# Performance work log

Hardware: AMD Instinct MI355X
Metric: run time of the kernel (lower is better)

Reference implementation:

```python
import jax, jax.numpy as jnp
import numpy as np

HIDDEN = 256
NUM_CLASSES = 25
INPUT_DIM = 76


def _lstm_layer(x, Wi, Wh, b):
    """Flax OptimizedLSTMCell semantics: gates [i, f, g, o], zero-init carry.
    x: [B, T, D]; Wi: [D, 4H]; Wh: [H, 4H]; b: [4H]. Returns hidden seq [B, T, H]."""
    B = x.shape[0]
    H = Wh.shape[0]
    c0 = jnp.zeros((B, H), x.dtype)
    h0 = jnp.zeros((B, H), x.dtype)

    def step(carry, xt):
        c, h = carry
        z = xt @ Wi + h @ Wh + b  # [B, 4H]
        i, f, g, o = jnp.split(z, 4, axis=-1)
        i = jax.nn.sigmoid(i)
        f = jax.nn.sigmoid(f)
        g = jnp.tanh(g)
        o = jax.nn.sigmoid(o)
        c = f * c + i * g
        h = o * jnp.tanh(c)
        return (c, h), h

    (_, _), ys = jax.lax.scan(step, (c0, h0), jnp.swapaxes(x, 0, 1))  # scan over time
    return jnp.swapaxes(ys, 0, 1)  # [B, T, H]


def setup_inputs() -> dict:
    key = jax.random.key(0)
    ks = jax.random.split(key, 9)
    B, T, D, H = 512, 512, INPUT_DIM, HIDDEN
    s_in = 1.0 / np.sqrt(D)
    s_h = 1.0 / np.sqrt(H)
    return {
        "x": jax.random.normal(ks[0], (B, T, D), jnp.float32),
        "Wi1": jax.random.normal(ks[1], (D, 4 * H), jnp.float32) * s_in,
        "Wh1": jax.random.normal(ks[2], (H, 4 * H), jnp.float32) * s_h,
        "b1": jnp.zeros((4 * H,), jnp.float32),
        "Wi2": jax.random.normal(ks[3], (H, 4 * H), jnp.float32) * s_h,
        "Wh2": jax.random.normal(ks[4], (H, 4 * H), jnp.float32) * s_h,
        "b2": jnp.zeros((4 * H,), jnp.float32),
        "Wd": jax.random.normal(ks[5], (H, NUM_CLASSES), jnp.float32) * s_h,
        "bd": jnp.zeros((NUM_CLASSES,), jnp.float32),
    }


def reference(x, Wi1, Wh1, b1, Wi2, Wh2, b2, Wd, bd):
    h1 = _lstm_layer(x, Wi1, Wh1, b1)   # [B, T, H]
    h2 = _lstm_layer(h1, Wi2, Wh2, b2)  # [B, T, H]
    feats = h2[:, -1]                   # dropout deterministic (eval mode)
    logits = feats @ Wd + bd            # [B, num_classes]
    return logits
```

## Files before the change

### kernel.cpp

```cpp
#include <hip/hip_runtime.h>

#define BB 512
#define TT 512
#define DD 76
#define HH 256
#define NC 25
#define NBLK 256
#define NTHREADS 512
#define BBHH (BB * HH)

#define K1 352
#define K2 512
#define WS1 360
#define WS2 520

typedef unsigned short u16;
typedef unsigned int u32;
typedef unsigned long long u64;
typedef __attribute__((ext_vector_type(8))) short bf16x8;
typedef __attribute__((ext_vector_type(4))) float f32x4;

__device__ __forceinline__ float bf2f(u16 v) {
  union { u32 u; float f; } c; c.u = ((u32)v) << 16; return c.f;
}
__device__ __forceinline__ u16 f2bf(float f) {
  union { u32 u; float f; } c; c.f = f;
  u32 r = c.u + 0x7FFFu + ((c.u >> 16) & 1u);
  return (u16)(r >> 16);
}
__device__ __forceinline__ void split2(float f, u16& h, u16& l) {
  u16 hh = f2bf(f);
  float r = f - bf2f(hh);
  h = hh; l = f2bf(r);
}
__device__ __forceinline__ float tanh_f(float v) {
  float e = __expf(2.0f * v);
  return 1.0f - 2.0f / (e + 1.0f);
}
__device__ __forceinline__ float gact(float v, bool is_tanh) {
  float e = __expf(is_tanh ? 2.0f * v : -v);
  float inv = 1.0f / (1.0f + e);
  return is_tanh ? 1.0f - 2.0f * inv : inv;
}

__device__ __forceinline__ u64 ald2(const u32* p) {
  return __hip_atomic_load((const u64*)p, __ATOMIC_RELAXED, __HIP_MEMORY_SCOPE_AGENT);
}
__device__ __forceinline__ u32 ald1(const u32* p) {
  return __hip_atomic_load(p, __ATOMIC_RELAXED, __HIP_MEMORY_SCOPE_AGENT);
}
__device__ __forceinline__ void ast1(u32* p, u32 v) {
  __hip_atomic_store(p, v, __ATOMIC_RELAXED, __HIP_MEMORY_SCOPE_AGENT);
}
__device__ __forceinline__ void ast2(u64* p, u64 v) {
  __hip_atomic_store(p, v, __ATOMIC_RELAXED, __HIP_MEMORY_SCOPE_AGENT);
}

__device__ __forceinline__ void wait_flags(const u32* fbase, u32 target) {
  if (threadIdx.x < 32) {
    const u32* p = fbase + threadIdx.x * 32;
    while (__hip_atomic_load(p, __ATOMIC_RELAXED, __HIP_MEMORY_SCOPE_AGENT) < target)
      __builtin_amdgcn_s_sleep(1);
  }
  __syncthreads();
}
__device__ __forceinline__ void post_flag(u32* slot, u32 val) {
  __syncthreads();
  if (threadIdx.x == 0) ast1(slot, val);
}

__device__ __forceinline__ bf16x8 hi8(const u64 w[4]) {
  union { u32 u[4]; bf16x8 v; } c;
#pragma unroll
  for (int i = 0; i < 4; ++i)
    c.u[i] = __builtin_amdgcn_perm((u32)(w[i] >> 32), (u32)w[i], 0x05040100u);
  return c.v;
}
__device__ __forceinline__ bf16x8 lo8(const u64 w[4]) {
  union { u32 u[4]; bf16x8 v; } c;
#pragma unroll
  for (int i = 0; i < 4; ++i)
    c.u[i] = __builtin_amdgcn_perm((u32)(w[i] >> 32), (u32)w[i], 0x07060302u);
  return c.v;
}

__device__ __forceinline__ void splitv8(const float* f, bf16x8& vh, bf16x8& vl) {
  union { u16 s[8]; bf16x8 v; } ch, cl;
#pragma unroll
  for (int i = 0; i < 8; ++i) { u16 h_, l_; split2(f[i], h_, l_); ch.s[i] = h_; cl.s[i] = l_; }
  vh = ch.v; vl = cl.v;
}

__global__ void repack_kernel(const float* __restrict__ Wi1, const float* __restrict__ Wh1,
                              const float* __restrict__ Wi2, const float* __restrict__ Wh2,
                              u16* __restrict__ w1hg, u16* __restrict__ w1lg,
                              u16* __restrict__ w2hg, u16* __restrict__ w2lg) {
  int idx = blockIdx.x * blockDim.x + threadIdx.x;
  const int N1 = 1024 * K1;
  if (idx < N1) {
    int c = idx / K1, k = idx - c * K1;
    int src = (c & 3) * HH + (c >> 2);
    float v = 0.f;
    if (k < HH) v = Wh1[k * 1024 + src];
    else if (k < HH + DD) v = Wi1[(k - HH) * 1024 + src];
    u16 h, l; split2(v, h, l);
    w1hg[idx] = h; w1lg[idx] = l;
  } else if (idx < N1 + 1024 * K2) {
    int d = idx - N1;
    int c = d >> 9, k = d & 511;
    int src = (c & 3) * HH + (c >> 2);
    float v = (k < HH) ? Wi2[k * 1024 + src] : Wh2[(k - HH) * 1024 + src];
    u16 h, l; split2(v, h, l);
    w2hg[d] = h; w2lg[d] = l;
  }
}

#define MFMA_CH6(AH, AL, PH0, PL0, PH1, PL1, KOFF, A0, B0, C0, A1, B1, C1)  \
  { bf16x8 b0h_ = *(const bf16x8*)((PH0) + (KOFF));                         \
    bf16x8 b0l_ = *(const bf16x8*)((PL0) + (KOFF));                         \
    bf16x8 b1h_ = *(const bf16x8*)((PH1) + (KOFF));                         \
    bf16x8 b1l_ = *(const bf16x8*)((PL1) + (KOFF));                         \
    A0 = __builtin_amdgcn_mfma_f32_16x16x32_bf16(AH, b0h_, A0, 0, 0, 0);    \
    B0 = __builtin_amdgcn_mfma_f32_16x16x32_bf16(AH, b0l_, B0, 0, 0, 0);    \
    C0 = __builtin_amdgcn_mfma_f32_16x16x32_bf16(AL, b0h_, C0, 0, 0, 0);    \
    A1 = __builtin_amdgcn_mfma_f32_16x16x32_bf16(AH, b1h_, A1, 0, 0, 0);    \
    B1 = __builtin_amdgcn_mfma_f32_16x16x32_bf16(AH, b1l_, B1, 0, 0, 0);    \
    C1 = __builtin_amdgcn_mfma_f32_16x16x32_bf16(AL, b1h_, C1, 0, 0, 0); }

#define GATES_ST(Z, CS, DST)                                                \
  { u32 hwv[4];                                                             \
    _Pragma("unroll")                                                       \
    for (int r = 0; r < 4; ++r) {                                           \
      float a_ = gact((Z)[r], gi == 2);                                     \
      float v1_ = __shfl_xor(a_, 1);                                        \
      float v2_ = __shfl_xor(a_, 2);                                        \
      float v3_ = __shfl_xor(a_, 3);                                        \
      float cn_ = v1_ * (CS)[r] + a_ * v2_;                                 \
      (CS)[r] = cn_;                                                        \
      float hv_ = v3_ * tanh_f(cn_);                                        \
      u16 hh_, hl_; split2(hv_, hh_, hl_);                                  \
      hwv[r] = (u32)hh_ | ((u32)hl_ << 16);                                 \
    }                                                                       \
    _Pragma("unroll")                                                       \
    for (int r = 0; r < 4; ++r) {                                           \
      int base_ = lane & 48;                                                \
      u32 w1_ = __shfl(hwv[r], base_ + 4);                                  \
      u32 w2_ = __shfl(hwv[r], base_ + 8);                                  \
      u32 w3_ = __shfl(hwv[r], base_ + 12);                                 \
      if (nl == 0) {                                                        \
        u64* dp_ = (u64*)((DST) + (size_t)(rbase + r) * HH + jt * 8 + kh * 4); \
        ast2(dp_,     (u64)hwv[r] | ((u64)w1_ << 32));                      \
        ast2(dp_ + 1, (u64)w2_    | ((u64)w3_ << 32));                      \
      }                                                                     \
    }                                                                       \
  }

#define LOAD_RW(RW, BASEPTR)                                                \
  { const u32* hp_ = (BASEPTR) + (size_t)arow * HH + kh * 128;              \
    _Pragma("unroll")                                                       \
    for (int i_ = 0; i_ < 4; ++i_) {                                        \
      const u32* p_ = hp_ + i_ * 32 + qd * 8;                               \
      (RW)[i_][0] = ald2(p_);     (RW)[i_][1] = ald2(p_ + 2);               \
      (RW)[i_][2] = ald2(p_ + 4); (RW)[i_][3] = ald2(p_ + 6);               \
    } }

__global__ __launch_bounds__(NTHREADS) void lstm_kernel(
    const float* __restrict__ x,
    const float* __restrict__ b1, const float* __restrict__ b2,
    const float* __restrict__ Wd, const float* __restrict__ bd,
    const u16* __restrict__ w1hg, const u16* __restrict__ w1lg,
    const u16* __restrict__ w2hg, const u16* __restrict__ w2lg,
    u32* __restrict__ h1w, u32* __restrict__ h2w,
    u32* __restrict__ flags,
    float* __restrict__ out)
{
  __shared__ u16 w1h[32 * WS1], w1l[32 * WS1];
  __shared__ u16 w2h[32 * WS2], w2l[32 * WS2];
  __shared__ float zx[2][8][64][4];

  const int tid = threadIdx.x;
  const int lane = tid & 63;
  const int wv = tid >> 6;
  const int m  = wv & 3;
  const int kh = wv >> 2;
  const int nl = lane & 15;
  const int qd = lane >> 4;
  const int bt = blockIdx.x & 7;
  const int jt = blockIdx.x >> 3;
  const int row0 = bt * 64;

  u32* fCp = flags + bt * 1024;
  u32* fCslot = fCp + jt * 32;

  for (int i = tid; i < 32 * (K1 / 2); i += NTHREADS) {
    int c = i / 176, kk = i - c * 176;
    ((u32*)&w1h[c * WS1])[kk] = ((const u32*)(w1hg + (size_t)(jt * 32 + c) * K1))[kk];
    ((u32*)&w1l[c * WS1])[kk] = ((const u32*)(w1lg + (size_t)(jt * 32 + c) * K1))[kk];
  }
  for (int i = tid; i < 32 * (K2 / 2); i += NTHREADS) {
    int c = i >> 8, kk = i & 255;
    ((u32*)&w2h[c * WS2])[kk] = ((const u32*)(w2hg + (size_t)(jt * 32 + c) * K2))[kk];
    ((u32*)&w2l[c * WS2])[kk] = ((const u32*)(w2lg + (size_t)(jt * 32 + c) * K2))[kk];
  }

  const int cg_col = jt * 32 + kh * 16 + nl;
  const int gi = cg_col & 3;
  const int rbase = row0 + m * 16 + qd * 4;
  const int arow = row0 + m * 16 + nl;

  float ab1[2], ab2[2];
#pragma unroll
  for (int tl = 0; tl < 2; ++tl) {
    int col = jt * 32 + tl * 16 + nl;
    float v1 = b1[(col & 3) * HH + (col >> 2)];
    float v2 = b2[(col & 3) * HH + (col >> 2)];
    ab1[tl] = (kh == 0) ? v1 : 0.f;
    ab2[tl] = (kh == 0) ? v2 : 0.f;
  }

  const u16* pB1h0 = w1h + nl * WS1;
  const u16* pB1l0 = w1l + nl * WS1;
  const u16* pB1h1 = w1h + (16 + nl) * WS1;
  const u16* pB1l1 = w1l + (16 + nl) * WS1;
  const u16* pB2h0 = w2h + nl * WS2;
  const u16* pB2l0 = w2l + nl * WS2;
  const u16* pB2h1 = w2h + (16 + nl) * WS2;
  const u16* pB2l1 = w2l + (16 + nl) * WS2;

  float cs1[4] = {0.f, 0.f, 0.f, 0.f}, cs2[4] = {0.f, 0.f, 0.f, 0.f};
  u64 rwh1[4][4], rw2[4][4];

  __syncthreads();

  {
    f32x4 aA0 = {ab1[0], ab1[0], ab1[0], ab1[0]};
    f32x4 aA1 = {ab1[1], ab1[1], ab1[1], ab1[1]};
    f32x4 aB0 = {0,0,0,0}, aB1 = {0,0,0,0}, aC0 = {0,0,0,0}, aC1 = {0,0,0,0};
    const float* xrow = x + (size_t)arow * TT * DD;
    if (kh == 0) {
#pragma unroll
      for (int ci = 0; ci < 2; ++ci) {
        float xv[8];
        float4 f0 = *(const float4*)(xrow + ci * 32 + qd * 8);
        float4 f1 = *(const float4*)(xrow + ci * 32 + qd * 8 + 4);
        xv[0]=f0.x; xv[1]=f0.y; xv[2]=f0.z; xv[3]=f0.w;
        xv[4]=f1.x; xv[5]=f1.y; xv[6]=f1.z; xv[7]=f1.w;
        bf16x8 xh, xl; splitv8(xv, xh, xl);
        const int koff = (8 + ci) * 32 + qd * 8;
        MFMA_CH6(xh, xl, pB1h0, pB1l0, pB1h1, pB1l1, koff, aA0, aB0, aC0, aA1, aB1, aC1)
      }
    } else {
      float xv[8] = {0,0,0,0,0,0,0,0};
      if (qd == 0) {
        float4 f0 = *(const float4*)(xrow + 64);
        float4 f1 = *(const float4*)(xrow + 68);
        xv[0]=f0.x; xv[1]=f0.y; xv[2]=f0.z; xv[3]=f0.w;
        xv[4]=f1.x; xv[5]=f1.y; xv[6]=f1.z; xv[7]=f1.w;
      } else if (qd == 1) {
        float4 f0 = *(const float4*)(xrow + 72);
        xv[0]=f0.x; xv[1]=f0.y; xv[2]=f0.z; xv[3]=f0.w;
      }
      bf16x8 xh, xl; splitv8(xv, xh, xl);
      const int koff = 10 * 32 + qd * 8;
      MFMA_CH6(xh, xl, pB1h0, pB1l0, pB1h1, pB1l1, koff, aA0, aB0, aC0, aA1, aB1, aC1)
    }
    f32x4 zk = (kh == 0) ? (aA0 + aB0 + aC0) : (aA1 + aB1 + aC1);
    f32x4 zo = (kh == 0) ? (aA1 + aB1 + aC1) : (aA0 + aB0 + aC0);
    *(f32x4*)&zx[1][wv][lane][0] = zo;
    __syncthreads();
    zk += *(const f32x4*)&zx[1][wv ^ 4][lane][0];
    GATES_ST(zk, cs1, h1w)
    post_flag(fCslot, 1u);
  }

#pragma unroll 1
  for (int t = 0; t < TT; ++t) {
    const u32* h1cw = h1w + (t & 1) * BBHH;
    u32* h1nw = h1w + ((t + 1) & 1) * BBHH;
    const u32* h2pw = h2w + ((t + 1) & 1) * BBHH;
    u32* h2cw = h2w + (t & 1) * BBHH;
    const bool doA = (t < TT - 1);

    f32x4 aA0 = {ab1[0], ab1[0], ab1[0], ab1[0]};
    f32x4 aA1 = {ab1[1], ab1[1], ab1[1], ab1[1]};
    f32x4 aB0 = {0,0,0,0}, aB1 = {0,0,0,0}, aC0 = {0,0,0,0}, aC1 = {0,0,0,0};
    f32x4 bA0 = {ab2[0], ab2[0], ab2[0], ab2[0]};
    f32x4 bA1 = {ab2[1], ab2[1], ab2[1], ab2[1]};
    f32x4 bB0 = {0,0,0,0}, bB1 = {0,0,0,0}, bC0 = {0,0,0,0}, bC1 = {0,0,0,0};

    float4 xf0, xf1, xf2, xf3;
    if (doA) {
      const float* xrow = x + ((size_t)arow * TT + (t + 1)) * DD;
      if (kh == 0) {
        xf0 = *(const float4*)(xrow + qd * 8);
        xf1 = *(const float4*)(xrow + qd * 8 + 4);
        xf2 = *(const float4*)(xrow + 32 + qd * 8);
        xf3 = *(const float4*)(xrow + 32 + qd * 8 + 4);
      } else {
        xf0 = make_float4(0,0,0,0); xf1 = make_float4(0,0,0,0);
        if (qd == 0) {
          xf0 = *(const float4*)(xrow + 64);
          xf1 = *(const float4*)(xrow + 68);
        } else if (qd == 1) {
          xf0 = *(const float4*)(xrow + 72);
        }
      }
    }

    wait_flags(fCp, (u32)(t + 1));

    LOAD_RW(rwh1, h1cw)
    if (t > 0) LOAD_RW(rw2, h2pw)

    if (doA) {
      float xv[8]; bf16x8 xh, xl;
      if (kh == 0) {
        xv[0]=xf0.x; xv[1]=xf0.y; xv[2]=xf0.z; xv[3]=xf0.w;
        xv[4]=xf1.x; xv[5]=xf1.y; xv[6]=xf1.z; xv[7]=xf1.w;
        splitv8(xv, xh, xl);
        MFMA_CH6(xh, xl, pB1h0, pB1l0, pB1h1, pB1l1, 8 * 32 + qd * 8,
                 aA0, aB0, aC0, aA1, aB1, aC1)
        xv[0]=xf2.x; xv[1]=xf2.y; xv[2]=xf2.z; xv[3]=xf2.w;
        xv[4]=xf3.x; xv[5]=xf3.y; xv[6]=xf3.z; xv[7]=xf3.w;
        splitv8(xv, xh, xl);
        MFMA_CH6(xh, xl, pB1h0, pB1l0, pB1h1, pB1l1, 9 * 32 + qd * 8,
                 aA0, aB0, aC0, aA1, aB1, aC1)
      } else {
        xv[0]=xf0.x; xv[1]=xf0.y; xv[2]=xf0.z; xv[3]=xf0.w;
        xv[4]=xf1.x; xv[5]=xf1.y; xv[6]=xf1.z; xv[7]=xf1.w;
        splitv8(xv, xh, xl);
        MFMA_CH6(xh, xl, pB1h0, pB1l0, pB1h1, pB1l1, 10 * 32 + qd * 8,
                 aA0, aB0, aC0, aA1, aB1, aC1)
      }
    }

#pragma unroll
    for (int i = 0; i < 4; ++i) {
      bf16x8 fh = hi8(rwh1[i]), fl = lo8(rwh1[i]);
      const int koff = (kh * 4 + i) * 32 + qd * 8;
      if (doA)
        MFMA_CH6(fh, fl, pB1h0, pB1l0, pB1h1, pB1l1, koff, aA0, aB0, aC0, aA1, aB1, aC1)
      MFMA_CH6(fh, fl, pB2h0, pB2l0, pB2h1, pB2l1, koff, bA0, bB0, bC0, bA1, bB1, bC1)
    }
    if (t > 0) {
#pragma unroll
      for (int i = 0; i < 4; ++i) {
        bf16x8 fh = hi8(rw2[i]), fl = lo8(rw2[i]);
        const int koff = (8 + kh * 4 + i) * 32 + qd * 8;
        MFMA_CH6(fh, fl, pB2h0, pB2l0, pB2h1, pB2l1, koff, bA0, bB0, bC0, bA1, bB1, bC1)
      }
    }

    f32x4 z2k = (kh == 0) ? (bA0 + bB0 + bC0) : (bA1 + bB1 + bC1);
    f32x4 z2o = (kh == 0) ? (bA1 + bB1 + bC1) : (bA0 + bB0 + bC0);
    *(f32x4*)&zx[0][wv][lane][0] = z2o;
    f32x4 z1k = {0,0,0,0};
    if (doA) {
      z1k = (kh == 0) ? (aA0 + aB0 + aC0) : (aA1 + aB1 + aC1);
      f32x4 z1o = (kh == 0) ? (aA1 + aB1 + aC1) : (aA0 + aB0 + aC0);
      *(f32x4*)&zx[1][wv][lane][0] = z1o;
    }
    __syncthreads();
    z2k += *(const f32x4*)&zx[0][wv ^ 4][lane][0];
    if (doA) {
      z1k += *(const f32x4*)&zx[1][wv ^ 4][lane][0];
      GATES_ST(z1k, cs1, h1nw)
    }
    GATES_ST(z2k, cs2, h2cw)
    post_flag(fCslot, (u32)(t + 2));
  }

  wait_flags(fCp, TT + 1);
  if (tid < 2 * NC) {
    int r = row0 + jt * 2 + tid / NC;
    int n = tid - (tid / NC) * NC;
    float s = bd[n];
    const u32* fw = h2w + BBHH + (size_t)r * HH;
#pragma unroll 8
    for (int k = 0; k < HH; ++k) {
      u32 w = ald1(fw + k);
      s += (bf2f((u16)w) + bf2f((u16)(w >> 16))) * Wd[k * NC + n];
    }
    out[r * NC + n] = s;
  }
}

extern "C" void kernel_launch(void* const* d_in, const int* in_sizes, int n_in,
                              void* d_out, int out_size, void* d_ws, size_t ws_size,
                              hipStream_t stream) {
  const float* x   = (const float*)d_in[0];
  const float* Wi1 = (const float*)d_in[1];
  const float* Wh1 = (const float*)d_in[2];
  const float* b1  = (const float*)d_in[3];
  const float* Wi2 = (const float*)d_in[4];
  const float* Wh2 = (const float*)d_in[5];
  const float* b2  = (const float*)d_in[6];
  const float* Wd  = (const float*)d_in[7];
  const float* bd  = (const float*)d_in[8];

  char* ws = (char*)d_ws;
  u32* h1w = (u32*)(ws);
  u32* h2w = (u32*)(ws + 1048576u);
  u16* w1hg = (u16*)(ws + 2097152u);
  u16* w1lg = (u16*)(ws + 2097152u + 720896u);
  u16* w2hg = (u16*)(ws + 2097152u + 2u * 720896u);
  u16* w2lg = (u16*)(ws + 2097152u + 2u * 720896u + 1048576u);
  u32* flags = (u32*)(ws + 5636096u);
  float* out = (float*)d_out;

  hipMemsetAsync((void*)flags, 0, 65536, stream);
  const int total = 1024 * K1 + 1024 * K2;
  repack_kernel<<<(total + 255) / 256, 256, 0, stream>>>(
      Wi1, Wh1, Wi2, Wh2, w1hg, w1lg, w2hg, w2lg);

  void* args[] = {
    (void*)&x, (void*)&b1, (void*)&b2, (void*)&Wd, (void*)&bd,
    (void*)&w1hg, (void*)&w1lg, (void*)&w2hg, (void*)&w2lg,
    (void*)&h1w, (void*)&h2w,
    (void*)&flags, (void*)&out
  };
  (void)hipLaunchCooperativeKernel((void*)lstm_kernel, dim3(NBLK),
                                   dim3(NTHREADS), args, 0, stream);
}
```

Baseline: 5.481 ms.

## Split LSTM work over 512 cooperative blocks with 16 gate columns each

Adds a new persistent kernel that runs 512 blocks, each owning 16 gate columns instead of 32. This halves the per-block MFMA and LDS weight footprint in each time step. The two K-halves of the block now finish different layers: kh==0 applies the layer-1 gates and kh==1 the layer-2 gates, so the elementwise gate work runs in parallel. The cost is polling 64 flags per row tile instead of 32 and tighter register limits from launch_bounds(512,4). The old 256-block kernel stays as a fallback if the cooperative launch fails.

```diff
diff --git a/kernel.cpp b/kernel.cpp
--- a/kernel.cpp
+++ b/kernel.cpp
@@ -5,7 +5,6 @@
 #define DD 76
 #define HH 256
 #define NC 25
-#define NBLK 256
 #define NTHREADS 512
 #define BBHH (BB * HH)
 
@@ -56,7 +55,15 @@
   __hip_atomic_store(p, v, __ATOMIC_RELAXED, __HIP_MEMORY_SCOPE_AGENT);
 }
 
-__device__ __forceinline__ void wait_flags(const u32* fbase, u32 target) {
+__device__ __forceinline__ void wait_flags64(const u32* fbase, u32 target) {
+  if (threadIdx.x < 64) {
+    const u32* p = fbase + threadIdx.x * 32;
+    while (__hip_atomic_load(p, __ATOMIC_RELAXED, __HIP_MEMORY_SCOPE_AGENT) < target)
+      __builtin_amdgcn_s_sleep(1);
+  }
+  __syncthreads();
+}
+__device__ __forceinline__ void wait_flags32(const u32* fbase, u32 target) {
   if (threadIdx.x < 32) {
     const u32* p = fbase + threadIdx.x * 32;
     while (__hip_atomic_load(p, __ATOMIC_RELAXED, __HIP_MEMORY_SCOPE_AGENT) < target)
@@ -85,10 +92,13 @@
 }
 
 __device__ __forceinline__ void splitv8(const float* f, bf16x8& vh, bf16x8& vl) {
-  union { u16 s[8]; bf16x8 v; } ch, cl;
-#pragma unroll
-  for (int i = 0; i < 8; ++i) { u16 h_, l_; split2(f[i], h_, l_); ch.s[i] = h_; cl.s[i] = l_; }
-  vh = ch.v; vl = cl.v;
+  union { u16 s[8]; bf16x8 v; } ch_, cl_;
+#pragma unroll
+  for (int i = 0; i < 8; ++i) {
+    u16 h_, l_; split2(f[i], h_, l_);
+    ch_.s[i] = h_; cl_.s[i] = l_;
+  }
+  vh = ch_.v; vl = cl_.v;
 }
 
 __global__ void repack_kernel(const float* __restrict__ Wi1, const float* __restrict__ Wh1,
@@ -115,6 +125,13 @@
   }
 }
 
+#define MCH3(AH, AL, PH, PL, KOFF, A, B, C)                                 \
+  { bf16x8 bh_ = *(const bf16x8*)((PH) + (KOFF));                           \
+    bf16x8 bl_ = *(const bf16x8*)((PL) + (KOFF));                           \
+    A = __builtin_amdgcn_mfma_f32_16x16x32_bf16(AH, bh_, A, 0, 0, 0);       \
+    B = __builtin_amdgcn_mfma_f32_16x16x32_bf16(AH, bl_, B, 0, 0, 0);       \
+    C = __builtin_amdgcn_mfma_f32_16x16x32_bf16(AL, bh_, C, 0, 0, 0); }
+
 #define MFMA_CH6(AH, AL, PH0, PL0, PH1, PL1, KOFF, A0, B0, C0, A1, B1, C1)  \
   { bf16x8 b0h_ = *(const bf16x8*)((PH0) + (KOFF));                         \
     bf16x8 b0l_ = *(const bf16x8*)((PL0) + (KOFF));                         \
@@ -127,7 +144,35 @@
     B1 = __builtin_amdgcn_mfma_f32_16x16x32_bf16(AH, b1l_, B1, 0, 0, 0);    \
     C1 = __builtin_amdgcn_mfma_f32_16x16x32_bf16(AL, b1h_, C1, 0, 0, 0); }
 
-#define GATES_ST(Z, CS, DST)                                                \
+#define GST16(Z, CS, DST)                                                   \
+  { u32 hwv[4];                                                             \
+    _Pragma("unroll")                                                       \
+    for (int r = 0; r < 4; ++r) {                                           \
+      float a_ = gact((Z)[r], gi == 2);                                     \
+      float v1_ = __shfl_xor(a_, 1);                                        \
+      float v2_ = __shfl_xor(a_, 2);                                        \
+      float v3_ = __shfl_xor(a_, 3);                                        \
+      float cn_ = v1_ * (CS)[r] + a_ * v2_;                                 \
+      (CS)[r] = cn_;                                                        \
+      float hv_ = v3_ * tanh_f(cn_);                                        \
+      u16 hh_, hl_; split2(hv_, hh_, hl_);                                  \
+      hwv[r] = (u32)hh_ | ((u32)hl_ << 16);                                 \
+    }                                                                       \
+    _Pragma("unroll")                                                       \
+    for (int r = 0; r < 4; ++r) {                                           \
+      int base_ = lane & 48;                                                \
+      u32 w1_ = __shfl(hwv[r], base_ + 4);                                  \
+      u32 w2_ = __shfl(hwv[r], base_ + 8);                                  \
+      u32 w3_ = __shfl(hwv[r], base_ + 12);                                 \
+      if (nl == 0) {                                                        \
+        u64* dp_ = (u64*)((DST) + (size_t)(rbase + r) * HH + jt * 4);       \
+        ast2(dp_,     (u64)hwv[r] | ((u64)w1_ << 32));                      \
+        ast2(dp_ + 1, (u64)w2_    | ((u64)w3_ << 32));                      \
+      }                                                                     \
+    }                                                                       \
+  }
+
+#define GST32(Z, CS, DST)                                                   \
   { u32 hwv[4];                                                             \
     _Pragma("unroll")                                                       \
     for (int r = 0; r < 4; ++r) {                                           \
@@ -164,7 +209,7 @@
       (RW)[i_][2] = ald2(p_ + 4); (RW)[i_][3] = ald2(p_ + 6);               \
     } }
 
-__global__ __launch_bounds__(NTHREADS) void lstm_kernel(
+__global__ __launch_bounds__(NTHREADS, 4) void lstm_kernel_a(
     const float* __restrict__ x,
     const float* __restrict__ b1, const float* __restrict__ b2,
     const float* __restrict__ Wd, const float* __restrict__ bd,
@@ -174,9 +219,9 @@
     u32* __restrict__ flags,
     float* __restrict__ out)
 {
-  __shared__ u16 w1h[32 * WS1], w1l[32 * WS1];
-  __shared__ u16 w2h[32 * WS2], w2l[32 * WS2];
-  __shared__ float zx[2][8][64][4];
+  __shared__ u16 w1h[16 * WS1], w1l[16 * WS1];
+  __shared__ u16 w2h[16 * WS2], w2l[16 * WS2];
+  __shared__ f32x4 zx[2][8][64];
 
   const int tid = threadIdx.x;
   const int lane = tid & 63;
@@ -189,53 +234,42 @@
   const int jt = blockIdx.x >> 3;
   const int row0 = bt * 64;
 
-  u32* fCp = flags + bt * 1024;
+  u32* fCp = flags + bt * 2048;
   u32* fCslot = fCp + jt * 32;
 
-  for (int i = tid; i < 32 * (K1 / 2); i += NTHREADS) {
+  for (int i = tid; i < 16 * (K1 / 2); i += NTHREADS) {
     int c = i / 176, kk = i - c * 176;
-    ((u32*)&w1h[c * WS1])[kk] = ((const u32*)(w1hg + (size_t)(jt * 32 + c) * K1))[kk];
-    ((u32*)&w1l[c * WS1])[kk] = ((const u32*)(w1lg + (size_t)(jt * 32 + c) * K1))[kk];
-  }
-  for (int i = tid; i < 32 * (K2 / 2); i += NTHREADS) {
+    ((u32*)&w1h[c * WS1])[kk] = ((const u32*)(w1hg + (size_t)(jt * 16 + c) * K1))[kk];
+    ((u32*)&w1l[c * WS1])[kk] = ((const u32*)(w1lg + (size_t)(jt * 16 + c) * K1))[kk];
+  }
+  for (int i = tid; i < 16 * (K2 / 2); i += NTHREADS) {
     int c = i >> 8, kk = i & 255;
-    ((u32*)&w2h[c * WS2])[kk] = ((const u32*)(w2hg + (size_t)(jt * 32 + c) * K2))[kk];
-    ((u32*)&w2l[c * WS2])[kk] = ((const u32*)(w2lg + (size_t)(jt * 32 + c) * K2))[kk];
-  }
-
-  const int cg_col = jt * 32 + kh * 16 + nl;
+    ((u32*)&w2h[c * WS2])[kk] = ((const u32*)(w2hg + (size_t)(jt * 16 + c) * K2))[kk];
+    ((u32*)&w2l[c * WS2])[kk] = ((const u32*)(w2lg + (size_t)(jt * 16 + c) * K2))[kk];
+  }
+
+  const int cg_col = jt * 16 + nl;
   const int gi = cg_col & 3;
   const int rbase = row0 + m * 16 + qd * 4;
   const int arow = row0 + m * 16 + nl;
 
-  float ab1[2], ab2[2];
-#pragma unroll
-  for (int tl = 0; tl < 2; ++tl) {
-    int col = jt * 32 + tl * 16 + nl;
-    float v1 = b1[(col & 3) * HH + (col >> 2)];
-    float v2 = b2[(col & 3) * HH + (col >> 2)];
-    ab1[tl] = (kh == 0) ? v1 : 0.f;
-    ab2[tl] = (kh == 0) ? v2 : 0.f;
-  }
-
-  const u16* pB1h0 = w1h + nl * WS1;
-  const u16* pB1l0 = w1l + nl * WS1;
-  const u16* pB1h1 = w1h + (16 + nl) * WS1;
-  const u16* pB1l1 = w1l + (16 + nl) * WS1;
-  const u16* pB2h0 = w2h + nl * WS2;
-  const u16* pB2l0 = w2l + nl * WS2;
-  const u16* pB2h1 = w2h + (16 + nl) * WS2;
-  const u16* pB2l1 = w2l + (16 + nl) * WS2;
-
-  float cs1[4] = {0.f, 0.f, 0.f, 0.f}, cs2[4] = {0.f, 0.f, 0.f, 0.f};
+  const float ab1 = (kh == 0) ? b1[gi * HH + (cg_col >> 2)] : 0.f;
+  const float ab2 = (kh == 0) ? b2[gi * HH + (cg_col >> 2)] : 0.f;
+
+  const u16* pB1h = w1h + nl * WS1;
+  const u16* pB1l = w1l + nl * WS1;
+  const u16* pB2h = w2h + nl * WS2;
+  const u16* pB2l = w2l + nl * WS2;
+
+  float cs1[4] = {0.f, 0.f, 0.f, 0.f};
+  float cs2[4] = {0.f, 0.f, 0.f, 0.f};
   u64 rwh1[4][4], rw2[4][4];
 
   __syncthreads();
 
   {
-    f32x4 aA0 = {ab1[0], ab1[0], ab1[0], ab1[0]};
-    f32x4 aA1 = {ab1[1], ab1[1], ab1[1], ab1[1]};
-    f32x4 aB0 = {0,0,0,0}, aB1 = {0,0,0,0}, aC0 = {0,0,0,0}, aC1 = {0,0,0,0};
+    f32x4 aA = {ab1, ab1, ab1, ab1};
+    f32x4 aB = {0,0,0,0}, aC = {0,0,0,0};
     const float* xrow = x + (size_t)arow * TT * DD;
     if (kh == 0) {
 #pragma unroll
@@ -246,8 +280,7 @@
         xv[0]=f0.x; xv[1]=f0.y; xv[2]=f0.z; xv[3]=f0.w;
         xv[4]=f1.x; xv[5]=f1.y; xv[6]=f1.z; xv[7]=f1.w;
         bf16x8 xh, xl; splitv8(xv, xh, xl);
-        const int koff = (8 + ci) * 32 + qd * 8;
-        MFMA_CH6(xh, xl, pB1h0, pB1l0, pB1h1, pB1l1, koff, aA0, aB0, aC0, aA1, aB1, aC1)
+        MCH3(xh, xl, pB1h, pB1l, (8 + ci) * 32 + qd * 8, aA, aB, aC)
       }
     } else {
       float xv[8] = {0,0,0,0,0,0,0,0};
@@ -261,15 +294,15 @@
         xv[0]=f0.x; xv[1]=f0.y; xv[2]=f0.z; xv[3]=f0.w;
       }
       bf16x8 xh, xl; splitv8(xv, xh, xl);
-      const int koff = 10 * 32 + qd * 8;
-      MFMA_CH6(xh, xl, pB1h0, pB1l0, pB1h1, pB1l1, koff, aA0, aB0, aC0, aA1, aB1, aC1)
-    }
-    f32x4 zk = (kh == 0) ? (aA0 + aB0 + aC0) : (aA1 + aB1 + aC1);
-    f32x4 zo = (kh == 0) ? (aA1 + aB1 + aC1) : (aA0 + aB0 + aC0);
-    *(f32x4*)&zx[1][wv][lane][0] = zo;
+      MCH3(xh, xl, pB1h, pB1l, 10 * 32 + qd * 8, aA, aB, aC)
+    }
+    f32x4 z1p = aA + aB + aC;
+    zx[1][wv][lane] = z1p;
     __syncthreads();
-    zk += *(const f32x4*)&zx[1][wv ^ 4][lane][0];
-    GATES_ST(zk, cs1, h1w)
+    if (kh == 0) {
+      f32x4 z1 = z1p + zx[1][wv ^ 4][lane];
+      GST16(z1, cs1, h1w)
+    }
     post_flag(fCslot, 1u);
   }
 
@@ -281,12 +314,10 @@
     u32* h2cw = h2w + (t & 1) * BBHH;
     const bool doA = (t < TT - 1);
 
-    f32x4 aA0 = {ab1[0], ab1[0], ab1[0], ab1[0]};
-    f32x4 aA1 = {ab1[1], ab1[1], ab1[1], ab1[1]};
-    f32x4 aB0 = {0,0,0,0}, aB1 = {0,0,0,0}, aC0 = {0,0,0,0}, aC1 = {0,0,0,0};
-    f32x4 bA0 = {ab2[0], ab2[0], ab2[0], ab2[0]};
-    f32x4 bA1 = {ab2[1], ab2[1], ab2[1], ab2[1]};
-    f32x4 bB0 = {0,0,0,0}, bB1 = {0,0,0,0}, bC0 = {0,0,0,0}, bC1 = {0,0,0,0};
+    f32x4 aA = {ab1, ab1, ab1, ab1};
+    f32x4 aB = {0,0,0,0}, aC = {0,0,0,0};
+    f32x4 bA = {ab2, ab2, ab2, ab2};
+    f32x4 bB = {0,0,0,0}, bC = {0,0,0,0};
 
     float4 xf0, xf1, xf2, xf3;
     if (doA) {
@@ -307,7 +338,224 @@
       }
     }
 
-    wait_flags(fCp, (u32)(t + 1));
+    wait_flags64(fCp, (u32)(t + 1));
+
+    LOAD_RW(rwh1, h1cw)
+    if (t > 0) LOAD_RW(rw2, h2pw)
+
+    if (doA) {
+      float xv[8]; bf16x8 xh, xl;
+      if (kh == 0) {
+        xv[0]=xf0.x; xv[1]=xf0.y; xv[2]=xf0.z; xv[3]=xf0.w;
+        xv[4]=xf1.x; xv[5]=xf1.y; xv[6]=xf1.z; xv[7]=xf1.w;
+        splitv8(xv, xh, xl);
+        MCH3(xh, xl, pB1h, pB1l, 8 * 32 + qd * 8, aA, aB, aC)
+        xv[0]=xf2.x; xv[1]=xf2.y; xv[2]=xf2.z; xv[3]=xf2.w;
+        xv[4]=xf3.x; xv[5]=xf3.y; xv[6]=xf3.z; xv[7]=xf3.w;
+        splitv8(xv, xh, xl);
+        MCH3(xh, xl, pB1h, pB1l, 9 * 32 + qd * 8, aA, aB, aC)
+      } else {
+        xv[0]=xf0.x; xv[1]=xf0.y; xv[2]=xf0.z; xv[3]=xf0.w;
+        xv[4]=xf1.x; xv[5]=xf1.y; xv[6]=xf1.z; xv[7]=xf1.w;
+        splitv8(xv, xh, xl);
+        MCH3(xh, xl, pB1h, pB1l, 10 * 32 + qd * 8, aA, aB, aC)
+      }
+    }
+
+#pragma unroll
+    for (int i = 0; i < 4; ++i) {
+      bf16x8 fh = hi8(rwh1[i]), fl = lo8(rwh1[i]);
+      const int koff = (kh * 4 + i) * 32 + qd * 8;
+      if (doA) MCH3(fh, fl, pB1h, pB1l, koff, aA, aB, aC)
+      MCH3(fh, fl, pB2h, pB2l, koff, bA, bB, bC)
+    }
+    if (t > 0) {
+#pragma unroll
+      for (int i = 0; i < 4; ++i) {
+        bf16x8 fh = hi8(rw2[i]), fl = lo8(rw2[i]);
+        MCH3(fh, fl, pB2h, pB2l, (8 + kh * 4 + i) * 32 + qd * 8, bA, bB, bC)
+      }
+    }
+
+    f32x4 z2p = bA + bB + bC;
+    zx[0][wv][lane] = z2p;
+    f32x4 z1p = {0,0,0,0};
+    if (doA) {
+      z1p = aA + aB + aC;
+      zx[1][wv][lane] = z1p;
+    }
+    __syncthreads();
+    if (kh == 0) {
+      if (doA) {
+        f32x4 z1 = z1p + zx[1][wv ^ 4][lane];
+        GST16(z1, cs1, h1nw)
+      }
+    } else {
+      f32x4 z2 = z2p + zx[0][wv ^ 4][lane];
+      GST16(z2, cs2, h2cw)
+    }
+    post_flag(fCslot, (u32)(t + 2));
+  }
+
+  wait_flags64(fCp, TT + 1);
+  if (tid < NC) {
+    int r = row0 + jt;
+    int n = tid;
+    float s = bd[n];
+    const u32* fw = h2w + BBHH + (size_t)r * HH;
+#pragma unroll 8
+    for (int k = 0; k < HH; ++k) {
+      u32 w = ald1(fw + k);
+      s += (bf2f((u16)w) + bf2f((u16)(w >> 16))) * Wd[k * NC + n];
+    }
+    out[r * NC + n] = s;
+  }
+}
+
+__global__ __launch_bounds__(NTHREADS) void lstm_kernel_b(
+    const float* __restrict__ x,
+    const float* __restrict__ b1, const float* __restrict__ b2,
+    const float* __restrict__ Wd, const float* __restrict__ bd,
+    const u16* __restrict__ w1hg, const u16* __restrict__ w1lg,
+    const u16* __restrict__ w2hg, const u16* __restrict__ w2lg,
+    u32* __restrict__ h1w, u32* __restrict__ h2w,
+    u32* __restrict__ flags,
+    float* __restrict__ out)
+{
+  __shared__ u16 w1h[32 * WS1], w1l[32 * WS1];
+  __shared__ u16 w2h[32 * WS2], w2l[32 * WS2];
+  __shared__ f32x4 zx[2][8][64];
+
+  const int tid = threadIdx.x;
+  const int lane = tid & 63;
+  const int wv = tid >> 6;
+  const int m  = wv & 3;
+  const int kh = wv >> 2;
+  const int nl = lane & 15;
+  const int qd = lane >> 4;
+  const int bt = blockIdx.x & 7;
+  const int jt = blockIdx.x >> 3;
+  const int row0 = bt * 64;
+
+  u32* fCp = flags + bt * 1024;
+  u32* fCslot = fCp + jt * 32;
+
+  for (int i = tid; i < 32 * (K1 / 2); i += NTHREADS) {
+    int c = i / 176, kk = i - c * 176;
+    ((u32*)&w1h[c * WS1])[kk] = ((const u32*)(w1hg + (size_t)(jt * 32 + c) * K1))[kk];
+    ((u32*)&w1l[c * WS1])[kk] = ((const u32*)(w1lg + (size_t)(jt * 32 + c) * K1))[kk];
+  }
+  for (int i = tid; i < 32 * (K2 / 2); i += NTHREADS) {
+    int c = i >> 8, kk = i & 255;
+    ((u32*)&w2h[c * WS2])[kk] = ((const u32*)(w2hg + (size_t)(jt * 32 + c) * K2))[kk];
+    ((u32*)&w2l[c * WS2])[kk] = ((const u32*)(w2lg + (size_t)(jt * 32 + c) * K2))[kk];
+  }
+
+  const int cg_col = jt * 32 + kh * 16 + nl;
+  const int gi = cg_col & 3;
+  const int rbase = row0 + m * 16 + qd * 4;
+  const int arow = row0 + m * 16 + nl;
+
+  float ab1[2], ab2[2];
+#pragma unroll
+  for (int tl = 0; tl < 2; ++tl) {
+    int col = jt * 32 + tl * 16 + nl;
+    float v1 = b1[(col & 3) * HH + (col >> 2)];
+    float v2 = b2[(col & 3) * HH + (col >> 2)];
+    ab1[tl] = (kh == 0) ? v1 : 0.f;
+    ab2[tl] = (kh == 0) ? v2 : 0.f;
+  }
+
+  const u16* pB1h0 = w1h + nl * WS1;
+  const u16* pB1l0 = w1l + nl * WS1;
+  const u16* pB1h1 = w1h + (16 + nl) * WS1;
+  const u16* pB1l1 = w1l + (16 + nl) * WS1;
+  const u16* pB2h0 = w2h + nl * WS2;
+  const u16* pB2l0 = w2l + nl * WS2;
+  const u16* pB2h1 = w2h + (16 + nl) * WS2;
+  const u16* pB2l1 = w2l + (16 + nl) * WS2;
+
+  float cs1[4] = {0.f, 0.f, 0.f, 0.f}, cs2[4] = {0.f, 0.f, 0.f, 0.f};
+  u64 rwh1[4][4], rw2[4][4];
+
+  __syncthreads();
+
+  {
+    f32x4 aA0 = {ab1[0], ab1[0], ab1[0], ab1[0]};
+    f32x4 aA1 = {ab1[1], ab1[1], ab1[1], ab1[1]};
+    f32x4 aB0 = {0,0,0,0}, aB1 = {0,0,0,0}, aC0 = {0,0,0,0}, aC1 = {0,0,0,0};
+    const float* xrow = x + (size_t)arow * TT * DD;
+    if (kh == 0) {
+#pragma unroll
+      for (int ci = 0; ci < 2; ++ci) {
+        float xv[8];
+        float4 f0 = *(const float4*)(xrow + ci * 32 + qd * 8);
+        float4 f1 = *(const float4*)(xrow + ci * 32 + qd * 8 + 4);
+        xv[0]=f0.x; xv[1]=f0.y; xv[2]=f0.z; xv[3]=f0.w;
+        xv[4]=f1.x; xv[5]=f1.y; xv[6]=f1.z; xv[7]=f1.w;
+        bf16x8 xh, xl; splitv8(xv, xh, xl);
+        const int koff = (8 + ci) * 32 + qd * 8;
+        MFMA_CH6(xh, xl, pB1h0, pB1l0, pB1h1, pB1l1, koff, aA0, aB0, aC0, aA1, aB1, aC1)
+      }
+    } else {
+      float xv[8] = {0,0,0,0,0,0,0,0};
+      if (qd == 0) {
+        float4 f0 = *(const float4*)(xrow + 64);
+        float4 f1 = *(const float4*)(xrow + 68);
+        xv[0]=f0.x; xv[1]=f0.y; xv[2]=f0.z; xv[3]=f0.w;
+        xv[4]=f1.x; xv[5]=f1.y; xv[6]=f1.z; xv[7]=f1.w;
+      } else if (qd == 1) {
+        float4 f0 = *(const float4*)(xrow + 72);
+        xv[0]=f0.x; xv[1]=f0.y; xv[2]=f0.z; xv[3]=f0.w;
+      }
+      bf16x8 xh, xl; splitv8(xv, xh, xl);
+      const int koff = 10 * 32 + qd * 8;
+      MFMA_CH6(xh, xl, pB1h0, pB1l0, pB1h1, pB1l1, koff, aA0, aB0, aC0, aA1, aB1, aC1)
+    }
+    f32x4 zk = (kh == 0) ? (aA0 + aB0 + aC0) : (aA1 + aB1 + aC1);
+    f32x4 zo = (kh == 0) ? (aA1 + aB1 + aC1) : (aA0 + aB0 + aC0);
+    zx[1][wv][lane] = zo;
+    __syncthreads();
+    zk += zx[1][wv ^ 4][lane];
+    GST32(zk, cs1, h1w)
+    post_flag(fCslot, 1u);
+  }
+
+#pragma unroll 1
+  for (int t = 0; t < TT; ++t) {
+    const u32* h1cw = h1w + (t & 1) * BBHH;
+    u32* h1nw = h1w + ((t + 1) & 1) * BBHH;
+    const u32* h2pw = h2w + ((t + 1) & 1) * BBHH;
+    u32* h2cw = h2w + (t & 1) * BBHH;
+    const bool doA = (t < TT - 1);
+
+    f32x4 aA0 = {ab1[0], ab1[0], ab1[0], ab1[0]};
+    f32x4 aA1 = {ab1[1], ab1[1], ab1[1], ab1[1]};
+    f32x4 aB0 = {0,0,0,0}, aB1 = {0,0,0,0}, aC0 = {0,0,0,0}, aC1 = {0,0,0,0};
+    f32x4 bA0 = {ab2[0], ab2[0], ab2[0], ab2[0]};
+    f32x4 bA1 = {ab2[1], ab2[1], ab2[1], ab2[1]};
+    f32x4 bB0 = {0,0,0,0}, bB1 = {0,0,0,0}, bC0 = {0,0,0,0}, bC1 = {0,0,0,0};
+
+    float4 xf0, xf1, xf2, xf3;
+    if (doA) {
+      const float* xrow = x + ((size_t)arow * TT + (t + 1)) * DD;
+      if (kh == 0) {
+        xf0 = *(const float4*)(xrow + qd * 8);
+        xf1 = *(const float4*)(xrow + qd * 8 + 4);
+        xf2 = *(const float4*)(xrow + 32 + qd * 8);
+        xf3 = *(const float4*)(xrow + 32 + qd * 8 + 4);
+      } else {
+        xf0 = make_float4(0,0,0,0); xf1 = make_float4(0,0,0,0);
+        if (qd == 0) {
+          xf0 = *(const float4*)(xrow + 64);
+          xf1 = *(const float4*)(xrow + 68);
+        } else if (qd == 1) {
+          xf0 = *(const float4*)(xrow + 72);
+        }
+      }
+    }
+
+    wait_flags32(fCp, (u32)(t + 1));
 
     LOAD_RW(rwh1, h1cw)
     if (t > 0) LOAD_RW(rw2, h2pw)
@@ -353,24 +601,24 @@
 
     f32x4 z2k = (kh == 0) ? (bA0 + bB0 + bC0) : (bA1 + bB1 + bC1);
     f32x4 z2o = (kh == 0) ? (bA1 + bB1 + bC1) : (bA0 + bB0 + bC0);
-    *(f32x4*)&zx[0][wv][lane][0] = z2o;
+    zx[0][wv][lane] = z2o;
     f32x4 z1k = {0,0,0,0};
     if (doA) {
       z1k = (kh == 0) ? (aA0 + aB0 + aC0) : (aA1 + aB1 + aC1);
       f32x4 z1o = (kh == 0) ? (aA1 + aB1 + aC1) : (aA0 + aB0 + aC0);
-      *(f32x4*)&zx[1][wv][lane][0] = z1o;
+      zx[1][wv][lane] = z1o;
     }
     __syncthreads();
-    z2k += *(const f32x4*)&zx[0][wv ^ 4][lane][0];
+    z2k += zx[0][wv ^ 4][lane];
     if (doA) {
-      z1k += *(const f32x4*)&zx[1][wv ^ 4][lane][0];
-      GATES_ST(z1k, cs1, h1nw)
-    }
-    GATES_ST(z2k, cs2, h2cw)
+      z1k += zx[1][wv ^ 4][lane];
+      GST32(z1k, cs1, h1nw)
+    }
+    GST32(z2k, cs2, h2cw)
     post_flag(fCslot, (u32)(t + 2));
   }
 
-  wait_flags(fCp, TT + 1);
+  wait_flags32(fCp, TT + 1);
   if (tid < 2 * NC) {
     int r = row0 + jt * 2 + tid / NC;
     int n = tid - (tid / NC) * NC;
@@ -408,7 +656,7 @@
   u32* flags = (u32*)(ws + 5636096u);
   float* out = (float*)d_out;
 
-  hipMemsetAsync((void*)flags, 0, 65536, stream);
+  (void)hipMemsetAsync((void*)flags, 0, 65536, stream);
   const int total = 1024 * K1 + 1024 * K2;
   repack_kernel<<<(total + 255) / 256, 256, 0, stream>>>(
       Wi1, Wh1, Wi2, Wh2, w1hg, w1lg, w2hg, w2lg);
@@ -419,6 +667,10 @@
     (void*)&h1w, (void*)&h2w,
     (void*)&flags, (void*)&out
   };
-  (void)hipLaunchCooperativeKernel((void*)lstm_kernel, dim3(NBLK),
-                                   dim3(NTHREADS), args, 0, stream);
-}
+  hipError_t e = hipLaunchCooperativeKernel((void*)lstm_kernel_a, dim3(512),
+                                            dim3(NTHREADS), args, 0, stream);
+  if (e != hipSuccess) {
+    (void)hipLaunchCooperativeKernel((void*)lstm_kernel_b, dim3(256),
+                                     dim3(NTHREADS), args, 0, stream);
+  }
+}
```

After: 11.28 ms. +105.7%, slower.
